# Kernel tuning notes

Hardware: AMD Instinct MI355X
Metric: run time of the kernel (lower is better)

Reference implementation:

```python
import jax, jax.numpy as jnp
import numpy as np

M, N, D, L, DEPTH, WIDTH, BATCH = 64, 4096, 64, 32, 4, 256, 1024
WIN = 2 * L + 1


def setup_inputs() -> dict:
    key = jax.random.key(0)
    ks = jax.random.split(key, 5)
    u = jax.random.normal(ks[0], (BATCH, D), dtype=jnp.float32)
    # xavier-style scaled gaussians for weights, zeros for biases (matches torch init pattern)
    weight0 = jax.random.normal(ks[1], (M, WIDTH, D), dtype=jnp.float32) * (2.0 / (WIDTH + D)) ** 0.5
    bias0 = jnp.zeros((M, WIDTH, 1), dtype=jnp.float32)
    weight = jax.random.normal(ks[2], (DEPTH - 1, M, WIDTH, WIDTH), dtype=jnp.float32) * (1.0 / WIDTH) ** 0.5
    bias = jnp.zeros((DEPTH - 1, M, WIDTH, 1), dtype=jnp.float32)
    weight_final = jax.random.normal(ks[3], (M, WIN, WIDTH), dtype=jnp.float32) * (2.0 / (WIN + WIDTH)) ** 0.5
    bias_final = jnp.zeros((M, WIN, 1), dtype=jnp.float32)
    xi = jax.random.normal(ks[4], (M, N + 2 * L), dtype=jnp.float32) * (2.0 / (M + N + 2 * L)) ** 0.5
    return {"u": u, "weight0": weight0, "bias0": bias0, "weight": weight,
            "bias": bias, "weight_final": weight_final, "bias_final": bias_final, "xi": xi}


def reference(u, weight0, bias0, weight, bias, weight_final, bias_final, xi) -> jnp.ndarray:
    act = jax.nn.sigmoid
    # per-M shared MLP: u1 [M, width, batch]
    u1 = act(jnp.einsum('mwd,bd->mwb', weight0, u) + bias0)
    for i in range(weight.shape[0]):  # small fixed depth loop
        u1 = act(jnp.einsum('mwv,mvb->mwb', weight[i], u1) + bias[i])
    G = act(jnp.einsum('mjw,mwb->mjb', weight_final, u1) + bias_final)
    # sliding-window correlation: out[n, b] = sum_{m,j} xi[m, n+j] * G[m, j, b]
    win = G.shape[1]
    n_out = xi.shape[1] - (win - 1)
    idx = jnp.arange(n_out)[:, None] + jnp.arange(win)[None, :]
    xw = xi[:, idx]
    return jnp.einsum('mnj,mjb->nb', xw, G)  # [N, batch]
```

## Files before the change

### kernel.cpp

```cpp
#include <hip/hip_runtime.h>
#include <math.h>

typedef __attribute__((ext_vector_type(8))) short short8;
typedef __attribute__((ext_vector_type(4))) float floatx4;
typedef __attribute__((ext_vector_type(4))) unsigned short ushort4v;

__device__ __forceinline__ void load_lds16(const void* g, void* l) {
    __builtin_amdgcn_global_load_lds((const __attribute__((address_space(1))) void*)g,
                                     (__attribute__((address_space(3))) void*)l,
                                     16, 0, 0);
}

__device__ __forceinline__ unsigned short f2bf(float x) {
    union { float f; unsigned int u; } v; v.f = x;
    unsigned int r = v.u + 0x7fffu + ((v.u >> 16) & 1u);
    return (unsigned short)(r >> 16);
}

__device__ __forceinline__ unsigned int pack_bf(float f0, float f1) {
    union { float f; unsigned int u; } a, b;
    a.f = f0; b.f = f1;
    return __builtin_amdgcn_perm(b.u + 0x8000u, a.u + 0x8000u, 0x07060302u);
}

__device__ __forceinline__ float fast_exp2(float x) {
#if __has_builtin(__builtin_amdgcn_exp2f)
    return __builtin_amdgcn_exp2f(x);
#else
    return __expf(x * 0.69314718056f);
#endif
}

__device__ __forceinline__ float fast_rcp(float x) {
#if __has_builtin(__builtin_amdgcn_rcpf)
    return __builtin_amdgcn_rcpf(x);
#else
    return 1.0f / x;
#endif
}

#define NEG_LOG2E (-1.4426950408889634f)

__device__ __forceinline__ float sigm(float x) { return 1.0f / (1.0f + __expf(-x)); }

__global__ void prep(const float* __restrict__ w0, const float* __restrict__ w,
                     const float* __restrict__ wf, const float* __restrict__ xi,
                     unsigned short* __restrict__ w0d, unsigned short* __restrict__ wd,
                     unsigned short* __restrict__ wfd, unsigned int* __restrict__ xw) {
    const int bid = blockIdx.x;
    if (bid < 6656) {
        const bool is0 = bid < 512;
        const int c = (is0 ? bid : bid - 512) * 256 + threadIdx.x;
        const int cpm = is0 ? 2048 : 8192;
        const int Kk  = is0 ? 2 : 8;
        const int K   = Kk * 32;
        const int mm  = c / cpm;
        const int cm  = c - mm * cpm;
        const int rblk = cm / (Kk * 64);
        const int rem  = cm - rblk * (Kk * 64);
        const int kk   = rem >> 6;
        const int lane = rem & 63;
        const int r  = rblk * 16 + (lane & 15);
        const int k0 = kk * 32 + (lane >> 4) * 8;
        const float* srcp = (is0 ? w0 : w) + ((size_t)mm * 256 + r) * K + k0;
        unsigned short* dstp = (is0 ? w0d : wd) + (size_t)c * 8;
        float4 a = *(const float4*)srcp;
        float4 b = *(const float4*)(srcp + 4);
        short8 o = { (short)f2bf(a.x), (short)f2bf(a.y), (short)f2bf(a.z), (short)f2bf(a.w),
                     (short)f2bf(b.x), (short)f2bf(b.y), (short)f2bf(b.z), (short)f2bf(b.w) };
        *(short8*)dstp = o;
    } else if (bid < 7680) {
        const int c = (bid - 6656) * 256 + threadIdx.x;
        const int m  = c >> 12;
        const int cm = c & 4095;
        const int rblk = cm >> 9;
        const int rem  = cm & 511;
        const int kk   = rem >> 6;
        const int lane = rem & 63;
        const int r  = rblk * 16 + (lane & 15);
        const int k0 = kk * 32 + (lane >> 4) * 8;
        short8 o = {0,0,0,0,0,0,0,0};
        if (r < 65) {
            const float* srcp = wf + ((size_t)m * 65 + r) * 256 + k0;
            float4 a = *(const float4*)srcp;
            float4 b = *(const float4*)(srcp + 4);
            o = (short8){ (short)f2bf(a.x), (short)f2bf(a.y), (short)f2bf(a.z), (short)f2bf(a.w),
                          (short)f2bf(b.x), (short)f2bf(b.y), (short)f2bf(b.z), (short)f2bf(b.w) };
        }
        *(short8*)(wfd + (size_t)c * 8) = o;
    } else {
        const int n = bid - 7680;
        #pragma unroll
        for (int t = 0; t < 9; ++t) {
            const int idx = t * 256 + threadIdx.x;
            if (idx < 2176) {
                const int m = idx / 34;
                const int pos = idx - m * 34;
                const int j0 = pos * 2;
                const float* xim = xi + (size_t)m * 4160 + n;
                const float v0 = (j0 < 65) ? xim[j0] : 0.0f;
                const float v1 = (j0 + 1 < 65) ? xim[j0 + 1] : 0.0f;
                xw[(size_t)n * 2176 + idx] =
                    (unsigned int)f2bf(v0) | ((unsigned int)f2bf(v1) << 16);
            }
        }
    }
}

template<int K, int I>
__device__ __forceinline__ void mlp_mfma(
    const unsigned short* __restrict__ Wt, const unsigned short* src,
    int wave, int lane, floatx4 (*acc)[4])
{
    const int Kk = K / 32;
    const int quad = lane >> 4, l16 = lane & 15;
    const int rblk0 = wave * I;
    const floatx4 zero = {0.f, 0.f, 0.f, 0.f};
    #pragma unroll
    for (int i = 0; i < I; ++i)
        #pragma unroll
        for (int j = 0; j < 4; ++j) acc[i][j] = zero;

    #pragma unroll
    for (int kk = 0; kk < Kk; ++kk) {
        short8 af[I], bf[4];
        #pragma unroll
        for (int i = 0; i < I; ++i)
            af[i] = *(const short8*)&Wt[(size_t)(((rblk0 + i) * Kk + kk) * 64 + lane) * 8];
        #pragma unroll
        for (int j = 0; j < 4; ++j) {
            const int cb = j * 16 + l16;
            bf[j] = *(const short8*)&src[cb * K + (((kk * 4 + quad) ^ (cb & 7)) * 8)];
        }
        #pragma unroll
        for (int i = 0; i < I; ++i)
            #pragma unroll
            for (int j = 0; j < 4; ++j)
                acc[i][j] = __builtin_amdgcn_mfma_f32_16x16x32_bf16(af[i], bf[j], acc[i][j], 0, 0, 0);
    }
}

__device__ __forceinline__ void mlp_write(
    const float* __restrict__ bm, unsigned short* dst,
    int wave, int lane, floatx4 (*acc)[4])
{
    const int quad = lane >> 4, l16 = lane & 15;
    const int rbw = wave * 64;
    #pragma unroll
    for (int i = 0; i < 4; ++i) {
        const int rb = rbw + i * 16 + quad * 4;
        float c0 = bm[rb]     * NEG_LOG2E;
        float c1 = bm[rb + 1] * NEG_LOG2E;
        float c2 = bm[rb + 2] * NEG_LOG2E;
        float c3 = bm[rb + 3] * NEG_LOG2E;
        #pragma unroll
        for (int j = 0; j < 4; ++j) {
            const int cb = j * 16 + l16;
            float r0 = fast_rcp(1.0f + fast_exp2(fmaf(acc[i][j][0], NEG_LOG2E, c0)));
            float r1 = fast_rcp(1.0f + fast_exp2(fmaf(acc[i][j][1], NEG_LOG2E, c1)));
            float r2 = fast_rcp(1.0f + fast_exp2(fmaf(acc[i][j][2], NEG_LOG2E, c2)));
            float r3 = fast_rcp(1.0f + fast_exp2(fmaf(acc[i][j][3], NEG_LOG2E, c3)));
            uint2 o = { pack_bf(r0, r1), pack_bf(r2, r3) };
            *(uint2*)&dst[cb * 256 + (((rb >> 3) ^ (cb & 7)) * 8) + (rb & 7)] = o;
        }
    }
}

__global__ __launch_bounds__(256, 3)
void fused_mlp(const float* __restrict__ u,
               const unsigned short* __restrict__ w0_bf, const float* __restrict__ b0_,
               const unsigned short* __restrict__ w_bf,  const float* __restrict__ b_,
               const unsigned short* __restrict__ wf_bf, const float* __restrict__ bf_,
               unsigned short* __restrict__ Gflat) {
    __shared__ unsigned short X[64 * 256];

    const int bid = blockIdx.x;
    const int xcd = bid & 7, slot = bid >> 3;
    const int m  = (xcd << 3) + (slot >> 4);
    const int b0 = (slot & 15) << 6;
    const int tid = threadIdx.x, wave = tid >> 6, lane = tid & 63;

    {
        const int b = tid >> 2, dc = tid & 3;
        const float* up = u + (size_t)(b0 + b) * 64 + dc * 16;
        float4 v0 = *(const float4*)(up);
        float4 v1 = *(const float4*)(up + 4);
        float4 v2 = *(const float4*)(up + 8);
        float4 v3 = *(const float4*)(up + 12);
        uint4 p0 = { pack_bf(v0.x, v0.y), pack_bf(v0.z, v0.w),
                     pack_bf(v1.x, v1.y), pack_bf(v1.z, v1.w) };
        uint4 p1 = { pack_bf(v2.x, v2.y), pack_bf(v2.z, v2.w),
                     pack_bf(v3.x, v3.y), pack_bf(v3.z, v3.w) };
        *(uint4*)&X[b * 64 + (((dc * 2)     ^ (b & 7)) * 8)] = p0;
        *(uint4*)&X[b * 64 + (((dc * 2 + 1) ^ (b & 7)) * 8)] = p1;
    }
    __syncthreads();

    floatx4 acc[4][4];

    mlp_mfma<64, 4>(w0_bf + (size_t)m * 16384, X, wave, lane, acc);
    __syncthreads();
    mlp_write(b0_ + (size_t)m * 256, X, wave, lane, acc);
    __syncthreads();

    #pragma unroll 1
    for (int l = 0; l < 3; ++l) {
        mlp_mfma<256, 4>(w_bf + ((size_t)l * 64 + m) * 65536, X, wave, lane, acc);
        __syncthreads();
        mlp_write(b_ + ((size_t)l * 64 + m) * 256, X, wave, lane, acc);
        __syncthreads();
    }

    {
        floatx4 acf[2][4];
        mlp_mfma<256, 2>(wf_bf + (size_t)m * 32768, X, wave, lane, acf);
        const int quad = lane >> 4, l16 = lane & 15;
        const float* bm = bf_ + (size_t)m * 65;
        unsigned short* Gg = Gflat + (size_t)b0 * 4352 + m * 68;
        #pragma unroll
        for (int i = 0; i < 2; ++i) {
            const int rb = wave * 32 + i * 16 + quad * 4;
            if (rb < 68) {
                float c[4];
                #pragma unroll
                for (int rr = 0; rr < 4; ++rr)
                    c[rr] = (rb + rr < 65) ? bm[rb + rr] * NEG_LOG2E : 0.0f;
                #pragma unroll
                for (int j = 0; j < 4; ++j) {
                    const int cb = j * 16 + l16;
                    float r0 = fast_rcp(1.0f + fast_exp2(fmaf(acf[i][j][0], NEG_LOG2E, c[0])));
                    float r1 = fast_rcp(1.0f + fast_exp2(fmaf(acf[i][j][1], NEG_LOG2E, c[1])));
                    float r2 = fast_rcp(1.0f + fast_exp2(fmaf(acf[i][j][2], NEG_LOG2E, c[2])));
                    float r3 = fast_rcp(1.0f + fast_exp2(fmaf(acf[i][j][3], NEG_LOG2E, c[3])));
                    uint2 o = { pack_bf(r0, r1), pack_bf(r2, r3) };
                    *(uint2*)&Gg[(size_t)cb * 4352 + rb] = o;
                }
            }
        }
    }
}

__global__ __launch_bounds__(256, 3)
void contract_gemm(const unsigned short* __restrict__ XW,
                   const unsigned short* __restrict__ G,
                   float* __restrict__ P) {
    const int bid = blockIdx.x;
    const int xcd = bid & 7, slot = bid >> 3;
    const int kc  = slot >> 5;
    const int rst = slot & 31;
    const int r0 = ((xcd << 2) + (rst >> 3)) << 7;
    const int c0 = (rst & 7) << 7;
    const int kb = kc * 1088;
    float* Pc = P + (size_t)kc * 4096 * 1024;

    __shared__ unsigned short As[128 * 64];
    __shared__ unsigned short Bs[128 * 64];

    const int tid = threadIdx.x;
    const int wave = tid >> 6, lane = tid & 63;
    const int quad = lane >> 4, l16 = lane & 15;
    const int wr = (wave & 1) * 64;
    const int wc = (wave >> 1) * 64;
    const int srow = wave * 32 + (lane >> 3);
    const int spos = lane & 7;

    floatx4 acc[4][4];
    const floatx4 zero = {0.f, 0.f, 0.f, 0.f};
    #pragma unroll
    for (int i = 0; i < 4; ++i)
        #pragma unroll
        for (int j = 0; j < 4; ++j) acc[i][j] = zero;

    for (int k0 = kb; k0 < kb + 1088; k0 += 64) {
        #pragma unroll
        for (int t = 0; t < 4; ++t) {
            const int row = srow + t * 8;
            const int fc  = spos ^ (row & 7);
            load_lds16(XW + (size_t)(r0 + row) * 4352 + k0 + fc * 8,
                       &As[(wave * 32 + t * 8) * 64]);
            load_lds16(G + (size_t)(c0 + row) * 4352 + k0 + fc * 8,
                       &Bs[(wave * 32 + t * 8) * 64]);
        }
        __syncthreads();

        #pragma unroll
        for (int kk = 0; kk < 2; ++kk) {
            short8 af[4], bfr[4];
            #pragma unroll
            for (int i = 0; i < 4; ++i) {
                const int ra = wr + i * 16 + l16;
                af[i]  = *(const short8*)&As[ra * 64 + (((kk * 4 + quad) ^ (ra & 7)) * 8)];
                const int cb = wc + i * 16 + l16;
                bfr[i] = *(const short8*)&Bs[cb * 64 + (((kk * 4 + quad) ^ (cb & 7)) * 8)];
            }
            #pragma unroll
            for (int i = 0; i < 4; ++i)
                #pragma unroll
                for (int j = 0; j < 4; ++j)
                    acc[i][j] = __builtin_amdgcn_mfma_f32_16x16x32_bf16(af[i], bfr[j], acc[i][j], 0, 0, 0);
        }
        __syncthreads();
    }

    #pragma unroll
    for (int i = 0; i < 4; ++i) {
        const int rb = r0 + wr + i * 16 + quad * 4;
        #pragma unroll
        for (int rr = 0; rr < 4; ++rr)
            #pragma unroll
            for (int j = 0; j < 4; ++j) {
                const int col = c0 + wc + j * 16 + l16;
                Pc[(size_t)(rb + rr) * 1024 + col] = acc[i][j][rr];
            }
    }
}

__global__ void reduce4(const float* __restrict__ P, float* __restrict__ out) {
    const int i = blockIdx.x * 256 + threadIdx.x;
    const float4* p = (const float4*)P;
    float4 a = p[i], b = p[i + 1048576], c = p[i + 2097152], d = p[i + 3145728];
    ((float4*)out)[i] = (float4){ a.x + b.x + c.x + d.x, a.y + b.y + c.y + d.y,
                                  a.z + b.z + c.z + d.z, a.w + b.w + c.w + d.w };
}

extern "C" void kernel_launch(void* const* d_in, const int* in_sizes, int n_in,
                              void* d_out, int out_size, void* d_ws, size_t ws_size,
                              hipStream_t stream) {
    const float* u   = (const float*)d_in[0];
    const float* w0  = (const float*)d_in[1];
    const float* b0_ = (const float*)d_in[2];
    const float* w   = (const float*)d_in[3];
    const float* b   = (const float*)d_in[4];
    const float* wf  = (const float*)d_in[5];
    const float* bf_ = (const float*)d_in[6];
    const float* xi  = (const float*)d_in[7];
    float* out = (float*)d_out;

    unsigned short* w0_bf = (unsigned short*)d_ws;
    unsigned short* w_bf  = w0_bf + 1048576;
    unsigned short* wf_bf = w_bf  + 12582912;
    unsigned short* Gflat = wf_bf + 2097152;
    unsigned short* XW    = Gflat + 4456448;
    float*          P     = (float*)(XW + 17825792);

    prep<<<11776, 256, 0, stream>>>(w0, w, wf, xi, w0_bf, w_bf, wf_bf, (unsigned int*)XW);
    fused_mlp<<<1024, 256, 0, stream>>>(u, w0_bf, b0_, w_bf, b, wf_bf, bf_, Gflat);
    contract_gemm<<<1024, 256, 0, stream>>>(XW, Gflat, P);
    reduce4<<<4096, 256, 0, stream>>>(P, out);
}
```

Before: 232.3 us.

## Halve fused MLP batch tile to 32 and stage G output through LDS

The fused MLP block now handles 32 batch columns instead of 64, halving the accumulator registers and the LDS buffer. This doubles the grid to 2048 blocks and raises the launch-bounds occupancy target from 3 to 6. The final G tile is first written to LDS and then copied to global memory as contiguous 32-bit rows, replacing the scattered 8-byte global stores. The cost is that each weight matrix is now streamed from memory by twice as many blocks, for less MFMA reuse per weight load.

```diff
diff --git a/kernel.cpp b/kernel.cpp
--- a/kernel.cpp
+++ b/kernel.cpp
@@ -3,7 +3,6 @@
 
 typedef __attribute__((ext_vector_type(8))) short short8;
 typedef __attribute__((ext_vector_type(4))) float floatx4;
-typedef __attribute__((ext_vector_type(4))) unsigned short ushort4v;
 
 __device__ __forceinline__ void load_lds16(const void* g, void* l) {
     __builtin_amdgcn_global_load_lds((const __attribute__((address_space(1))) void*)g,
@@ -40,8 +39,6 @@
 }
 
 #define NEG_LOG2E (-1.4426950408889634f)
-
-__device__ __forceinline__ float sigm(float x) { return 1.0f / (1.0f + __expf(-x)); }
 
 __global__ void prep(const float* __restrict__ w0, const float* __restrict__ w,
                      const float* __restrict__ wf, const float* __restrict__ xi,
@@ -107,42 +104,45 @@
     }
 }
 
-template<int K, int I>
+template<int K, int I, int J>
 __device__ __forceinline__ void mlp_mfma(
     const unsigned short* __restrict__ Wt, const unsigned short* src,
-    int wave, int lane, floatx4 (*acc)[4])
+    int wave, int lane, floatx4 (*acc)[J])
 {
-    const int Kk = K / 32;
+    constexpr int Kk = K / 32;
     const int quad = lane >> 4, l16 = lane & 15;
     const int rblk0 = wave * I;
     const floatx4 zero = {0.f, 0.f, 0.f, 0.f};
     #pragma unroll
     for (int i = 0; i < I; ++i)
         #pragma unroll
-        for (int j = 0; j < 4; ++j) acc[i][j] = zero;
+        for (int j = 0; j < J; ++j) acc[i][j] = zero;
+
+    const unsigned short* wbase = Wt + (size_t)((rblk0 * Kk) * 64 + lane) * 8;
 
     #pragma unroll
     for (int kk = 0; kk < Kk; ++kk) {
-        short8 af[I], bf[4];
+        short8 a[I], bf[J];
         #pragma unroll
         for (int i = 0; i < I; ++i)
-            af[i] = *(const short8*)&Wt[(size_t)(((rblk0 + i) * Kk + kk) * 64 + lane) * 8];
-        #pragma unroll
-        for (int j = 0; j < 4; ++j) {
+            a[i] = *(const short8*)(wbase + (size_t)(i * Kk + kk) * 512);
+        #pragma unroll
+        for (int j = 0; j < J; ++j) {
             const int cb = j * 16 + l16;
             bf[j] = *(const short8*)&src[cb * K + (((kk * 4 + quad) ^ (cb & 7)) * 8)];
         }
         #pragma unroll
         for (int i = 0; i < I; ++i)
             #pragma unroll
-            for (int j = 0; j < 4; ++j)
-                acc[i][j] = __builtin_amdgcn_mfma_f32_16x16x32_bf16(af[i], bf[j], acc[i][j], 0, 0, 0);
-    }
-}
-
+            for (int j = 0; j < J; ++j)
+                acc[i][j] = __builtin_amdgcn_mfma_f32_16x16x32_bf16(a[i], bf[j], acc[i][j], 0, 0, 0);
+    }
+}
+
+template<int J>
 __device__ __forceinline__ void mlp_write(
     const float* __restrict__ bm, unsigned short* dst,
-    int wave, int lane, floatx4 (*acc)[4])
+    int wave, int lane, floatx4 (*acc)[J])
 {
     const int quad = lane >> 4, l16 = lane & 15;
     const int rbw = wave * 64;
@@ -154,7 +154,7 @@
         float c2 = bm[rb + 2] * NEG_LOG2E;
         float c3 = bm[rb + 3] * NEG_LOG2E;
         #pragma unroll
-        for (int j = 0; j < 4; ++j) {
+        for (int j = 0; j < J; ++j) {
             const int cb = j * 16 + l16;
             float r0 = fast_rcp(1.0f + fast_exp2(fmaf(acc[i][j][0], NEG_LOG2E, c0)));
             float r1 = fast_rcp(1.0f + fast_exp2(fmaf(acc[i][j][1], NEG_LOG2E, c1)));
@@ -166,57 +166,53 @@
     }
 }
 
-__global__ __launch_bounds__(256, 3)
+__global__ __launch_bounds__(256, 6)
 void fused_mlp(const float* __restrict__ u,
                const unsigned short* __restrict__ w0_bf, const float* __restrict__ b0_,
                const unsigned short* __restrict__ w_bf,  const float* __restrict__ b_,
                const unsigned short* __restrict__ wf_bf, const float* __restrict__ bf_,
                unsigned short* __restrict__ Gflat) {
-    __shared__ unsigned short X[64 * 256];
+    __shared__ unsigned short X[32 * 256];
 
     const int bid = blockIdx.x;
     const int xcd = bid & 7, slot = bid >> 3;
-    const int m  = (xcd << 3) + (slot >> 4);
-    const int b0 = (slot & 15) << 6;
+    const int m  = (xcd << 3) + (slot >> 5);
+    const int b0 = (slot & 31) << 5;
     const int tid = threadIdx.x, wave = tid >> 6, lane = tid & 63;
 
     {
-        const int b = tid >> 2, dc = tid & 3;
-        const float* up = u + (size_t)(b0 + b) * 64 + dc * 16;
+        const int b = tid >> 3, dc = tid & 7;
+        const float* up = u + (size_t)(b0 + b) * 64 + dc * 8;
         float4 v0 = *(const float4*)(up);
         float4 v1 = *(const float4*)(up + 4);
-        float4 v2 = *(const float4*)(up + 8);
-        float4 v3 = *(const float4*)(up + 12);
         uint4 p0 = { pack_bf(v0.x, v0.y), pack_bf(v0.z, v0.w),
                      pack_bf(v1.x, v1.y), pack_bf(v1.z, v1.w) };
-        uint4 p1 = { pack_bf(v2.x, v2.y), pack_bf(v2.z, v2.w),
-                     pack_bf(v3.x, v3.y), pack_bf(v3.z, v3.w) };
-        *(uint4*)&X[b * 64 + (((dc * 2)     ^ (b & 7)) * 8)] = p0;
-        *(uint4*)&X[b * 64 + (((dc * 2 + 1) ^ (b & 7)) * 8)] = p1;
+        *(uint4*)&X[b * 64 + ((dc ^ (b & 7)) * 8)] = p0;
     }
     __syncthreads();
 
-    floatx4 acc[4][4];
-
-    mlp_mfma<64, 4>(w0_bf + (size_t)m * 16384, X, wave, lane, acc);
+    floatx4 acc[4][2];
+
+    mlp_mfma<64, 4, 2>(w0_bf + (size_t)m * 16384, X, wave, lane, acc);
     __syncthreads();
-    mlp_write(b0_ + (size_t)m * 256, X, wave, lane, acc);
+    mlp_write<2>(b0_ + (size_t)m * 256, X, wave, lane, acc);
     __syncthreads();
 
     #pragma unroll 1
     for (int l = 0; l < 3; ++l) {
-        mlp_mfma<256, 4>(w_bf + ((size_t)l * 64 + m) * 65536, X, wave, lane, acc);
-        __syncthreads();
-        mlp_write(b_ + ((size_t)l * 64 + m) * 256, X, wave, lane, acc);
+        mlp_mfma<256, 4, 2>(w_bf + ((size_t)l * 64 + m) * 65536, X, wave, lane, acc);
+        __syncthreads();
+        mlp_write<2>(b_ + ((size_t)l * 64 + m) * 256, X, wave, lane, acc);
         __syncthreads();
     }
 
     {
-        floatx4 acf[2][4];
-        mlp_mfma<256, 2>(wf_bf + (size_t)m * 32768, X, wave, lane, acf);
+        floatx4 acf[2][2];
+        mlp_mfma<256, 2, 2>(wf_bf + (size_t)m * 32768, X, wave, lane, acf);
+        __syncthreads();
+        unsigned short* Gt = X;
         const int quad = lane >> 4, l16 = lane & 15;
         const float* bm = bf_ + (size_t)m * 65;
-        unsigned short* Gg = Gflat + (size_t)b0 * 4352 + m * 68;
         #pragma unroll
         for (int i = 0; i < 2; ++i) {
             const int rb = wave * 32 + i * 16 + quad * 4;
@@ -226,17 +222,24 @@
                 for (int rr = 0; rr < 4; ++rr)
                     c[rr] = (rb + rr < 65) ? bm[rb + rr] * NEG_LOG2E : 0.0f;
                 #pragma unroll
-                for (int j = 0; j < 4; ++j) {
+                for (int j = 0; j < 2; ++j) {
                     const int cb = j * 16 + l16;
                     float r0 = fast_rcp(1.0f + fast_exp2(fmaf(acf[i][j][0], NEG_LOG2E, c[0])));
                     float r1 = fast_rcp(1.0f + fast_exp2(fmaf(acf[i][j][1], NEG_LOG2E, c[1])));
                     float r2 = fast_rcp(1.0f + fast_exp2(fmaf(acf[i][j][2], NEG_LOG2E, c[2])));
                     float r3 = fast_rcp(1.0f + fast_exp2(fmaf(acf[i][j][3], NEG_LOG2E, c[3])));
                     uint2 o = { pack_bf(r0, r1), pack_bf(r2, r3) };
-                    *(uint2*)&Gg[(size_t)cb * 4352 + rb] = o;
+                    *(uint2*)&Gt[cb * 68 + rb] = o;
                 }
             }
         }
+        __syncthreads();
+        unsigned short* Gg = Gflat + (size_t)b0 * 4352 + m * 68;
+        const int row = tid >> 3, l8 = tid & 7;
+        const unsigned int* srcr = (const unsigned int*)&Gt[row * 68];
+        unsigned int* dstg = (unsigned int*)&Gg[(size_t)row * 4352];
+        #pragma unroll
+        for (int t = l8; t < 34; t += 8) dstg[t] = srcr[t];
     }
 }
 
@@ -344,7 +347,7 @@
     float*          P     = (float*)(XW + 17825792);
 
     prep<<<11776, 256, 0, stream>>>(w0, w, wf, xi, w0_bf, w_bf, wf_bf, (unsigned int*)XW);
-    fused_mlp<<<1024, 256, 0, stream>>>(u, w0_bf, b0_, w_bf, b, wf_bf, bf_, Gflat);
+    fused_mlp<<<2048, 256, 0, stream>>>(u, w0_bf, b0_, w_bf, b, wf_bf, bf_, Gflat);
     contract_gemm<<<1024, 256, 0, stream>>>(XW, Gflat, P);
     reduce4<<<4096, 256, 0, stream>>>(P, out);
 }
```

New measurement: 271.6 us. +16.9%, slower.
